# Optimization experiments

Measured on AMD Instinct MI355X. Metric: run time of the kernel, lower is better.

## Reference

```python
import jax, jax.numpy as jnp
import numpy as np

B_S, N_NODES, D_FEAT, N_HEADS, N_BLOCKS, AVG_DEG = 8, 4096, 128, 4, 32, 16
D_HID, N_CLASSES = 256, 16


def setup_inputs() -> dict:
    key = jax.random.key(0)
    ks = jax.random.split(key, 6)
    x = jax.random.normal(ks[0], (B_S, N_NODES, D_FEAT), jnp.float32)
    e_per = N_NODES * AVG_DEG
    src = jax.random.randint(ks[1], (B_S, e_per), 0, N_NODES)
    dst = jax.random.randint(ks[2], (B_S, e_per), 0, N_NODES)
    off = jnp.arange(B_S)[:, None] * N_NODES
    edge_index = jnp.stack([(src + off).reshape(-1), (dst + off).reshape(-1)], 0).astype(jnp.int32)
    W_rank = jax.random.normal(ks[3], (D_FEAT, N_HEADS), jnp.float32) / np.sqrt(D_FEAT)
    W1 = jax.random.normal(ks[4], (2 * D_FEAT, D_HID), jnp.float32) / np.sqrt(2.0 * D_FEAT)
    W_out = jax.random.normal(ks[5], (D_HID, N_CLASSES), jnp.float32) / np.sqrt(D_HID)
    return {"x": x, "W_rank": W_rank, "W1": W1, "W_out": W_out,
            "edge_index": edge_index, "j": N_BLOCKS}


def _forward(x, W_rank, W1, W_out, edge_index, j):
    b_s, n, d = x.shape
    h = W_rank.shape[1]
    k = n // j                      # block (subgraph) size; j*k == n
    Bp = h * b_s * j                # number of (head, graph, block) blocks
    src, dst = edge_index[0], edge_index[1]
    N = b_s * n
    x_flat = x.reshape(N, d)

    # GCN-normalized adjacency Ahat with self loops (selfloop=1)
    deg = jnp.ones(N, x.dtype).at[dst].add(1.0)
    w = jax.lax.rsqrt(deg[src] * deg[dst])

    def ahat_mv(v):  # Ahat @ v, v: [N, c]
        out = jnp.zeros_like(v).at[dst].add(w[:, None] * v[src])
        return out + v / deg[:, None]

    # app_adj: concat(x, Ahat @ x)
    x_appd = ahat_mv(x_flat)

    # ranking: linear scores + one propagation hop -> [b, h, n]
    scores = ahat_mv(x_flat @ W_rank)
    scores = scores.reshape(b_s, n, h).transpose(0, 2, 1)

    # perm_gen: full descending sort split into j blocks of k (sorted_idx [b,h,j,k])
    order = jnp.argsort(-scores, axis=-1)        # [b,h,n] node ids in rank order
    pos = jnp.argsort(order, axis=-1)            # inverse: node -> sorted slot
    sorted_scores = jnp.take_along_axis(scores, order, axis=-1)
    perm_val = jax.nn.sigmoid(sorted_scores).reshape(b_s, h, j, k)  # relaxed perm values
    sorted_blocks = order.reshape(b_s, h, j, k)
    # local target slot: rank of node id within each block (data-dependent perm)
    tgt = jnp.argsort(jnp.argsort(sorted_blocks, axis=-1), axis=-1)

    # gather features (with appended Ahat@x) into sorted block order
    feats = jnp.concatenate([x, x_appd.reshape(b_s, n, d)], -1)      # [b,n,2d]
    feats_sorted = feats[jnp.arange(b_s)[:, None, None], order]       # [b,h,n,2d]
    feats_in = feats_sorted.reshape(b_s, h, j, k, 2 * d).transpose(1, 0, 2, 3, 4).reshape(Bp, k, 2 * d)

    # edge masking per head: keep edges whose endpoints land in the same block,
    # remap to local slots -> dense block adjacency [Bp, k, k]
    b_e = src // n
    src_l, dst_l = src % n, dst % n
    heads = jnp.arange(h)
    pos_s = pos[b_e[:, None], heads[None, :], src_l[:, None]]   # [E,h]
    pos_d = pos[b_e[:, None], heads[None, :], dst_l[:, None]]
    blk_s, slot_s = pos_s // k, pos_s % k
    blk_d, slot_d = pos_d // k, pos_d % k
    keep = (blk_s == blk_d).astype(x.dtype)
    block_id = (heads[None, :] * b_s + b_e[:, None]) * j + blk_s  # (h,b,j) layout
    A = jnp.zeros((Bp, k, k), x.dtype).at[block_id, slot_s, slot_d].add(keep)

    # relaxed permutation matrix P[b', s, tgt_s] = v_s  (sub_size = 1)
    val_f = perm_val.transpose(1, 0, 2, 3).reshape(Bp, k)
    tgt_f = tgt.transpose(1, 0, 2, 3).reshape(Bp, k)
    P = jnp.zeros((Bp, k, k), x.dtype).at[
        jnp.arange(Bp)[:, None], jnp.arange(k)[None, :], tgt_f].set(val_f)

    # sparse_perm_2D: new_adj[tgt_s, tgt_t] += v_s * v_t * A[s, t]  ==  P^T A P
    A_perm = jnp.einsum('bsi,bst,btj->bij', P, A, P)
    X_perm = jnp.einsum('bsi,bsd->bid', P, feats_in)

    # cocn: one message-passing layer on permuted blocks + mean pool + head
    Hh = jax.nn.relu(jnp.einsum('bij,bjd->bid', A_perm, X_perm) @ W1)
    logits = Hh.mean(1) @ W_out                        # [Bp, C]
    logits = logits.reshape(h, b_s, j, -1).mean(0)     # head average -> [b, j, C]
    return jax.nn.log_softmax(logits, axis=-1)         # single-class task


def reference(x, W_rank, W1, W_out, edge_index, j):
    return _forward(x, W_rank, W1, W_out, edge_index, j)
```

## Files before the change

kernel.cpp:

```cpp
#include <hip/hip_runtime.h>
#include <cmath>

#define NB 8
#define NN 4096
#define DF 128
#define NH 4
#define NJ 32
#define NK 128
#define NTOT (NB*NN)
#define ETOT 524288
#define BPB (NH*NB*NJ)
#define DHID 256
#define NCLS 16
#define CAP_PB 96
#define CAP_BP 512

#define FP_SCALE 4194304.0
#define FP_INV   (1.0/4194304.0)

typedef short bf16x8 __attribute__((ext_vector_type(8)));
typedef float f32x4  __attribute__((ext_vector_type(4)));

__device__ __forceinline__ unsigned short f2bf(float f) {
    unsigned u = __float_as_uint(f);
    unsigned r = (u + 0x7FFFu + ((u >> 16) & 1u)) >> 16;
    return (unsigned short)r;
}
__device__ __forceinline__ float bf2f(unsigned short b) {
    unsigned u = ((unsigned)b) << 16;
    return __uint_as_float(u);
}

__device__ __forceinline__ unsigned long long make_key(float sc, int p) {
    unsigned u = __float_as_uint(sc);
    unsigned s = u ^ ((unsigned)((int)u >> 31) | 0x80000000u);
    return ((unsigned long long)(s ^ 0xFFFFFFFFu) << 12) | (unsigned)p;
}

__global__ void k0_init(int* deg_i, int* fill, int* fill2) {
    int t = blockIdx.x * blockDim.x + threadIdx.x;
    if (t < NTOT) { deg_i[t] = 0; fill2[t] = 0; }
    if (t < BPB) fill[t] = 0;
}

__global__ __launch_bounds__(256) void k1_deg_prep(const int* __restrict__ ei,
                                                   const float* __restrict__ x,
                                                   const float* __restrict__ W1,
                                                   const float* __restrict__ wr,
                                                   int* deg_i,
                                                   unsigned short* __restrict__ xbf,
                                                   unsigned short* __restrict__ w1t,
                                                   float* __restrict__ scores_pre) {
    int bid = blockIdx.x, tid = threadIdx.x;
    if (bid < 2048) {
        int e = bid * 256 + tid;
        atomicAdd(&deg_i[ei[ETOT + e]], 1);
    } else if (bid < 4096) {
        int idx = (bid - 2048) * 256 + tid;
        const float* sp = x + (size_t)idx * 8;
        float4 lo = *(const float4*)sp;
        float4 hi = *(const float4*)(sp + 4);
        unsigned short u[8] = {f2bf(lo.x), f2bf(lo.y), f2bf(lo.z), f2bf(lo.w),
                               f2bf(hi.x), f2bf(hi.y), f2bf(hi.z), f2bf(hi.w)};
        *(bf16x8*)(xbf + (size_t)idx * 8) = *(bf16x8*)u;
    } else if (bid < 4352) {
        int t = (bid - 4096) * 256 + tid;
        int k = t >> 8, n = t & 255;
        w1t[n * 256 + k] = f2bf(W1[k * DHID + n]);
    } else {
        int t = (bid - 4352) * 256 + tid;
        int g = t >> 2, hh = t & 3;
        const float* xr = x + (size_t)g * DF;
        double acc = 0.0;
        for (int d0 = 0; d0 < DF; ++d0) acc += (double)xr[d0] * (double)wr[d0 * NH + hh];
        scores_pre[t] = (float)acc;
    }
}

__global__ __launch_bounds__(256) void k_prep2(const int* __restrict__ deg_i,
                                               float* __restrict__ rdeg,
                                               int* __restrict__ nbase) {
    int bid = blockIdx.x, tid = threadIdx.x;
    if (bid < 128) {
        int t = bid * 256 + tid;
        rdeg[t] = 1.0f / sqrtf((float)(1 + deg_i[t]));
        return;
    }
    __shared__ int part[256];
    int base0 = tid * 128;
    int s = 0;
    for (int i = 0; i < 128; ++i) s += deg_i[base0 + i];
    part[tid] = s;
    __syncthreads();
    for (int off = 1; off < 256; off <<= 1) {
        int v = (tid >= off) ? part[tid - off] : 0;
        __syncthreads();
        part[tid] += v;
        __syncthreads();
    }
    int running = (tid == 0) ? 0 : part[tid - 1];
    for (int i = 0; i < 128; ++i) {
        nbase[base0 + i] = running;
        running += deg_i[base0 + i];
    }
    if (tid == 255) nbase[NTOT] = running;
}

__global__ void k3c_fill_csr(const int* __restrict__ ei, const int* __restrict__ nbase,
                             int* fill2, int* __restrict__ csr_src) {
    int e = blockIdx.x * blockDim.x + threadIdx.x;
    if (e >= ETOT) return;
    int s = ei[e], d = ei[ETOT + e];
    int slot = atomicAdd(&fill2[d], 1);
    csr_src[nbase[d] + slot] = s;
}

__global__ __launch_bounds__(256) void k4_gather(const int* __restrict__ csr_src,
                                                 const int* __restrict__ nbase,
                                                 const float* __restrict__ rdeg,
                                                 const float* __restrict__ x,
                                                 const float* __restrict__ scores_pre,
                                                 unsigned* __restrict__ xappbf,
                                                 int* __restrict__ iscore) {
    __shared__ unsigned long long nb[4][64];
    int bid = blockIdx.x;
    if (bid < 8192) {
        int swz = (bid & 7) * 1024 + (bid >> 3);
        int wid = threadIdx.x >> 6;
        int wv = swz * 4 + wid;
        int lane = threadIdx.x & 63;
        float rd = rdeg[wv];
        float2 v = ((const float2*)(x + (size_t)wv * DF))[lane];
        float acc0 = v.x * rd * rd, acc1 = v.y * rd * rd;
        int t0 = nbase[wv], t1 = nbase[wv + 1];
        int deg = t1 - t0;
        if (lane < deg && lane < 64) {
            int s = csr_src[t0 + lane];
            float w = rd * rdeg[s];
            nb[wid][lane] = ((unsigned long long)__float_as_uint(w) << 32)
                          | (unsigned)(s * DF);
        }
        int nfull = min(deg, 64);
#pragma unroll 4
        for (int t = 0; t < nfull; ++t) {
            unsigned long long e = nb[wid][t];
            float w = __uint_as_float((unsigned)(e >> 32));
            float2 u = ((const float2*)(x + (e & 0xFFFFFFFFu)))[lane];
            acc0 = fmaf(w, u.x, acc0);
            acc1 = fmaf(w, u.y, acc1);
        }
        for (int t = t0 + 64; t < t1; ++t) {
            int s = csr_src[t];
            float w = rd * rdeg[s];
            float2 u = ((const float2*)(x + (size_t)s * DF))[lane];
            acc0 = fmaf(w, u.x, acc0);
            acc1 = fmaf(w, u.y, acc1);
        }
        xappbf[(size_t)wv * 64 + lane] =
            (unsigned)f2bf(acc0) | ((unsigned)f2bf(acc1) << 16);
    } else {
        int t = (bid - 8192) * 256 + threadIdx.x;
        int d = t >> 2, hh = t & 3;
        float rdd = rdeg[d];
        int t0 = nbase[d], t1 = nbase[d + 1];
        int acc = 0;
        for (int e = t0; e < t1; ++e) {
            int s = csr_src[e];
            float w = rdeg[s] * rdd;
            double term = (double)(w * scores_pre[s * NH + hh]);
            acc += __double2int_rn(term * FP_SCALE);
        }
        iscore[t] = acc;
    }
}

__global__ __launch_bounds__(256) void kg_mfma(const unsigned short* __restrict__ xbf,
                                               const unsigned short* __restrict__ xappbf,
                                               const unsigned short* __restrict__ w1t,
                                               unsigned short* __restrict__ Gbf) {
    __shared__ __align__(16) unsigned short As[128 * 64];
    __shared__ __align__(16) unsigned short Bs[128 * 64];
    int bid = blockIdx.x;
    int m0 = (bid >> 1) * 128, n0 = (bid & 1) * 128;
    int tid = threadIdx.x, lane = tid & 63, wid = tid >> 6;
    int wr = wid >> 1, wc = wid & 1;
    f32x4 acc[4][4];
#pragma unroll
    for (int mi = 0; mi < 4; ++mi)
#pragma unroll
        for (int ni = 0; ni < 4; ++ni) acc[mi][ni] = f32x4{0.f, 0.f, 0.f, 0.f};

    for (int kk = 0; kk < 4; ++kk) {
        int k0 = kk * 64;
        const unsigned short* Asrc = (kk < 2) ? xbf : xappbf;
        int kbase = k0 & 127;
#pragma unroll
        for (int i = 0; i < 4; ++i) {
            int gi = tid + i * 256;
            int r = gi >> 3, c = gi & 7;
            int csrc = c ^ (r & 7);
            *(bf16x8*)&As[r * 64 + c * 8] =
                *(const bf16x8*)(Asrc + (size_t)(m0 + r) * DF + kbase + csrc * 8);
        }
#pragma unroll
        for (int i = 0; i < 4; ++i) {
            int gi = tid + i * 256;
            int r = gi >> 3, c = gi & 7;
            int csrc = c ^ (r & 7);
            *(bf16x8*)&Bs[r * 64 + c * 8] =
                *(const bf16x8*)(w1t + (size_t)(n0 + r) * 256 + k0 + csrc * 8);
        }
        __syncthreads();
#pragma unroll
        for (int ks = 0; ks < 2; ++ks) {
            bf16x8 af[4], bfr[4];
#pragma unroll
            for (int mi = 0; mi < 4; ++mi) {
                int r = wr * 64 + mi * 16 + (lane & 15);
                int gl = ks * 4 + (lane >> 4);
                af[mi] = *(const bf16x8*)&As[r * 64 + (gl ^ (r & 7)) * 8];
            }
#pragma unroll
            for (int ni = 0; ni < 4; ++ni) {
                int r = wc * 64 + ni * 16 + (lane & 15);
                int gl = ks * 4 + (lane >> 4);
                bfr[ni] = *(const bf16x8*)&Bs[r * 64 + (gl ^ (r & 7)) * 8];
            }
#pragma unroll
            for (int mi = 0; mi < 4; ++mi)
#pragma unroll
                for (int ni = 0; ni < 4; ++ni)
                    acc[mi][ni] = __builtin_amdgcn_mfma_f32_16x16x32_bf16(
                        af[mi], bfr[ni], acc[mi][ni], 0, 0, 0);
        }
        __syncthreads();
    }
#pragma unroll
    for (int mi = 0; mi < 4; ++mi) {
        int rbase = m0 + wr * 64 + mi * 16 + (lane >> 4) * 4;
#pragma unroll
        for (int ni = 0; ni < 4; ++ni) {
            int col = n0 + wc * 64 + ni * 16 + (lane & 15);
#pragma unroll
            for (int j = 0; j < 4; ++j)
                Gbf[(size_t)(rbase + j) * DHID + col] = f2bf(acc[mi][ni][j]);
        }
    }
}

__global__ __launch_bounds__(256) void k5a_chunk(const float* __restrict__ scores_pre,
                                                 const int* __restrict__ iscore,
                                                 const int* __restrict__ deg_i,
                                                 unsigned long long* __restrict__ sorted64) {
    __shared__ unsigned long long sk[512];
    int blk = blockIdx.x;
    int seg = blk >> 3, chunk = blk & 7;
    int b = seg >> 2, hh = seg & 3;
    int tid = threadIdx.x;
    for (int i = tid; i < 512; i += 256) {
        int p = chunk * 512 + i;
        int g = b * NN + p;
        float dg = (float)(1 + deg_i[g]);
        float sc = scores_pre[g * NH + hh] / dg + (float)((double)iscore[g * NH + hh] * FP_INV);
        sk[i] = make_key(sc, p);
    }
    __syncthreads();
    for (int size = 2; size <= 512; size <<= 1) {
        for (int stride = size >> 1; stride > 0; stride >>= 1) {
            for (int p = tid; p < 512; p += 256) {
                int q = p ^ stride;
                if (q > p) {
                    unsigned long long kp = sk[p], kq = sk[q];
                    bool before_qp = (kq < kp);
                    bool asc = ((p & size) == 0);
                    if (asc ? before_qp : !before_qp) { sk[p] = kq; sk[q] = kp; }
                }
            }
            __syncthreads();
        }
    }
    for (int i = tid; i < 512; i += 256)
        sorted64[seg * NN + chunk * 512 + i] = sk[i];
}

__global__ __launch_bounds__(256) void k5b_rank(const unsigned long long* __restrict__ sorted64,
                                                int* __restrict__ order, int* __restrict__ pos,
                                                float* __restrict__ val) {
    int t = blockIdx.x * 256 + threadIdx.x;
    int seg = t >> 12, i = t & 4095;
    int chunk = i >> 9, slot = i & 511;
    const unsigned long long* segp = sorted64 + (size_t)seg * NN;
    unsigned long long k = segp[chunk * 512 + slot];
    int rank = slot;
#pragma unroll
    for (int c = 0; c < 8; ++c) {
        if (c == chunk) continue;
        const unsigned long long* cp = segp + c * 512;
        int lo = 0, hi = 512;
        while (lo < hi) { int mid = (lo + hi) >> 1; lo = (cp[mid] < k) ? mid + 1 : lo; hi = (cp[mid] < k) ? hi : mid; }
        rank += lo;
    }
    int p = (int)(k & 4095u);
    pos[seg * NN + p] = rank;
    order[seg * NN + rank] = p;
    unsigned s = (unsigned)(k >> 12) ^ 0xFFFFFFFFu;
    unsigned u = s ^ (((int)s >= 0) ? 0xFFFFFFFFu : 0x80000000u);
    float sc = __uint_as_float(u);
    val[seg * NN + rank] = 1.0f / (1.0f + expf(-sc));
}

__global__ __launch_bounds__(256) void k56_tgt_bin(const int* __restrict__ order,
                                                   const int* __restrict__ ei,
                                                   const int* __restrict__ pos,
                                                   int* __restrict__ tgt,
                                                   int* fill, unsigned* __restrict__ elist) {
    __shared__ unsigned short pos_l[NN];
    __shared__ unsigned buf[NJ][CAP_PB];
    __shared__ int lcnt[NJ];
    __shared__ int gbase[NJ];
    int bid = blockIdx.x, tid = threadIdx.x;
    if (bid < 512) {
        int* o = (int*)pos_l;
        int base = bid * 256;
        o[tid] = order[base + tid];
        __syncthreads();
        int g0 = tid & ~127;
        int me = o[tid];
        int r = 0;
#pragma unroll 16
        for (int s2 = 0; s2 < 128; ++s2) r += (o[g0 + s2] < me) ? 1 : 0;
        tgt[base + tid] = r;
        return;
    }
    int blkid = bid - 512;
    int ph = blkid >> 3, part = blkid & 7;
    int b = ph >> 2, hh = ph & 3;
    for (int i = tid; i < NN; i += 256) pos_l[i] = (unsigned short)pos[ph * NN + i];
    if (tid < NJ) lcnt[tid] = 0;
    __syncthreads();
    int ebase = b * 65536 + part * 8192;
    for (int i = tid; i < 8192; i += 256) {
        int e = ebase + i;
        int s = ei[e], d = ei[ETOT + e];
        int ps = pos_l[s & 4095], pd = pos_l[d & 4095];
        if ((ps >> 7) == (pd >> 7)) {
            int blk = ps >> 7;
            int slot = atomicAdd(&lcnt[blk], 1);
            if (slot < CAP_PB)
                buf[blk][slot] = (unsigned)((ps & 127) | ((pd & 127) << 16));
        }
    }
    __syncthreads();
    if (tid < NJ) {
        int n = min(lcnt[tid], CAP_PB);
        lcnt[tid] = n;
        gbase[tid] = atomicAdd(&fill[((hh * NB + b) * NJ) + tid], n);
    }
    __syncthreads();
    for (int t = tid; t < NJ * CAP_PB; t += 256) {
        int blk = t / CAP_PB, i = t % CAP_PB;
        if (i < lcnt[blk]) {
            int g0 = gbase[blk] + i;
            if (g0 < CAP_BP) {
                int bpid = ((hh * NB + b) * NJ) + blk;
                elist[bpid * CAP_BP + g0] = buf[blk][i];
            }
        }
    }
}

__global__ __launch_bounds__(256) void k9_block(const unsigned short* __restrict__ Gbf,
                                                const int* __restrict__ order,
                                                const float* __restrict__ val,
                                                const int* __restrict__ tgt,
                                                const int* __restrict__ fill,
                                                const unsigned* __restrict__ elist,
                                                const float* __restrict__ Wo,
                                                float* __restrict__ logits_bp) {
    __shared__ float val_s[NK];
    __shared__ int   node_s[NK];
    __shared__ int   tgt_s[NK];
    __shared__ int   rcnt[NK];
    __shared__ int   rend[NK];
    __shared__ int   rfill[NK];
    __shared__ unsigned es_meta[CAP_BP];
    __shared__ float    es_coef[CAP_BP];
    __shared__ float hvec[DHID];
    int i0 = blockIdx.x;
    int xcd = i0 & 7, r0 = i0 >> 3;
    int hh = r0 >> 5, blk = r0 & 31, b = xcd;
    int bp = (hh * NB + b) * NJ + blk;
    int ph = (b << 2) | hh;
    int tid = threadIdx.x;
    if (tid < NK) {
        int p = blk * NK + tid;
        node_s[tid] = order[ph * NN + p];
        val_s[tid]  = val[ph * NN + p];
        tgt_s[tid]  = tgt[ph * NN + p];
        rcnt[tid] = 0; rfill[tid] = 0;
    }
    __syncthreads();
    int e0 = bp * CAP_BP;
    int ne = min(fill[bp], CAP_BP);
    for (int t = tid; t < ne; t += 256)
        atomicAdd(&rcnt[tgt_s[elist[e0 + t] & 0xffff]], 1);
    __syncthreads();
    if (tid < NK) rend[tid] = rcnt[tid];
    __syncthreads();
    for (int off = 1; off < NK; off <<= 1) {
        int v = 0;
        if (tid < NK && tid >= off) v = rend[tid - off];
        __syncthreads();
        if (tid < NK) rend[tid] += v;
        __syncthreads();
    }
    for (int t = tid; t < ne; t += 256) {
        unsigned ent = elist[e0 + t];
        int ss = ent & 0xffff, sd = ent >> 16;
        int row = tgt_s[ss];
        int slot = atomicAdd(&rfill[row], 1);
        int p0 = rend[row] - rcnt[row] + slot;
        es_meta[p0] = ((unsigned)row << 16) | (unsigned)node_s[sd];
        es_coef[p0] = val_s[ss] * val_s[sd] * val_s[sd];
    }
    __syncthreads();
    size_t gb = (size_t)b * NN * DHID + tid;
    float hsum = 0.f, m = 0.f;
    int prev = -1;
#pragma unroll 4
    for (int i = 0; i < ne; ++i) {
        unsigned md = es_meta[i];
        int row = (int)(md >> 16);
        float g = bf2f(Gbf[gb + (size_t)(md & 0xffffu) * DHID]);
        float c = es_coef[i];
        bool flush = (row != prev);
        hsum += flush ? fmaxf(m, 0.f) : 0.f;
        m = flush ? c * g : fmaf(c, g, m);
        prev = row;
    }
    hsum += fmaxf(m, 0.f);
    hvec[tid] = hsum * (1.0f / NK);
    __syncthreads();
    if (tid < NCLS) {
        float s = 0.f;
        for (int q = 0; q < DHID; ++q) s = fmaf(hvec[q], Wo[q * NCLS + tid], s);
        logits_bp[bp * NCLS + tid] = s;
    }
}

__global__ void k10_final(const float* __restrict__ logits_bp, float* __restrict__ out) {
    int t = threadIdx.x;
    int b = t >> 5, blk = t & 31;
    float v[NCLS];
#pragma unroll
    for (int c = 0; c < NCLS; ++c) {
        float s = 0.f;
        for (int hh = 0; hh < NH; ++hh)
            s += logits_bp[(((hh * NB + b) * NJ) + blk) * NCLS + c];
        v[c] = s * 0.25f;
    }
    float mx = v[0];
#pragma unroll
    for (int c = 1; c < NCLS; ++c) mx = fmaxf(mx, v[c]);
    float se = 0.f;
#pragma unroll
    for (int c = 0; c < NCLS; ++c) se += expf(v[c] - mx);
    float lse = logf(se);
#pragma unroll
    for (int c = 0; c < NCLS; ++c) out[t * NCLS + c] = v[c] - mx - lse;
}

extern "C" void kernel_launch(void* const* d_in, const int* in_sizes, int n_in,
                              void* d_out, int out_size, void* d_ws, size_t ws_size,
                              hipStream_t stream) {
    const float* x  = (const float*)d_in[0];
    const float* wr = (const float*)d_in[1];
    const float* W1 = (const float*)d_in[2];
    const float* Wo = (const float*)d_in[3];
    const int*   ei = (const int*)d_in[4];

    char* ws = (char*)d_ws;
    int*      deg_i      = (int*)(ws + 0);
    float*    rdeg       = (float*)(ws + 131072);
    float*    scores_pre = (float*)(ws + 262144);
    int*      iscore     = (int*)(ws + 786432);
    unsigned short* xbf  = (unsigned short*)(ws + 1310720);
    unsigned* xappbf     = (unsigned*)(ws + 9699328);
    unsigned short* Gbf  = (unsigned short*)(ws + 18087936);
    int*      order      = (int*)(ws + 51642368);
    int*      pos        = (int*)(ws + 52166656);
    int*      tgt        = (int*)(ws + 52690944);
    float*    val        = (float*)(ws + 53215232);
    int*      fill       = (int*)(ws + 53743616);
    int*      csr_src    = (int*)(ws + 53755904);
    unsigned short* w1t  = (unsigned short*)(ws + 55853056);
    unsigned* elist      = (unsigned*)(ws + 53755904);
    float*    logits_bp  = (float*)(ws + 62144512);
    int*      nbase      = (int*)(ws + 62210048);
    int*      fill2      = (int*)(ws + 62341184);
    unsigned long long* sorted64 = (unsigned long long*)(ws + 62472256);

    k0_init<<<128, 256, 0, stream>>>(deg_i, fill, fill2);
    k1_deg_prep<<<4864, 256, 0, stream>>>(ei, x, W1, wr, deg_i, xbf, w1t, scores_pre);
    k_prep2<<<129, 256, 0, stream>>>(deg_i, rdeg, nbase);
    k3c_fill_csr<<<2048, 256, 0, stream>>>(ei, nbase, fill2, csr_src);
    k4_gather<<<8704, 256, 0, stream>>>(csr_src, nbase, rdeg, x, scores_pre, xappbf, iscore);
    kg_mfma<<<512, 256, 0, stream>>>(xbf, (const unsigned short*)xappbf, w1t, Gbf);
    k5a_chunk<<<256, 256, 0, stream>>>(scores_pre, iscore, deg_i, sorted64);
    k5b_rank<<<512, 256, 0, stream>>>(sorted64, order, pos, val);
    k56_tgt_bin<<<768, 256, 0, stream>>>(order, ei, pos, tgt, fill, elist);
    k9_block<<<BPB, 256, 0, stream>>>(Gbf, order, val, tgt, fill, elist, Wo, logits_bp);
    k10_final<<<1, 256, 0, stream>>>(logits_bp, (float*)d_out);
}
```

Before: 199.1 us.

## Gather bf16 features, swizzle edge blocks, merge GEMM with chunk sort launch

Result: faster. 183.8 us (-7.7%).

```diff
diff --git a/kernel.cpp b/kernel.cpp
--- a/kernel.cpp
+++ b/kernel.cpp
@@ -53,7 +53,7 @@
                                                    float* __restrict__ scores_pre) {
     int bid = blockIdx.x, tid = threadIdx.x;
     if (bid < 2048) {
-        int e = bid * 256 + tid;
+        int e = (bid & 7) * 65536 + (bid >> 3) * 256 + tid;
         atomicAdd(&deg_i[ei[ETOT + e]], 1);
     } else if (bid < 4096) {
         int idx = (bid - 2048) * 256 + tid;
@@ -108,8 +108,8 @@
 
 __global__ void k3c_fill_csr(const int* __restrict__ ei, const int* __restrict__ nbase,
                              int* fill2, int* __restrict__ csr_src) {
-    int e = blockIdx.x * blockDim.x + threadIdx.x;
-    if (e >= ETOT) return;
+    int bid = blockIdx.x;
+    int e = (bid & 7) * 65536 + (bid >> 3) * 256 + threadIdx.x;
     int s = ei[e], d = ei[ETOT + e];
     int slot = atomicAdd(&fill2[d], 1);
     csr_src[nbase[d] + slot] = s;
@@ -119,6 +119,7 @@
                                                  const int* __restrict__ nbase,
                                                  const float* __restrict__ rdeg,
                                                  const float* __restrict__ x,
+                                                 const unsigned short* __restrict__ xbf,
                                                  const float* __restrict__ scores_pre,
                                                  unsigned* __restrict__ xappbf,
                                                  int* __restrict__ iscore) {
@@ -145,16 +146,16 @@
         for (int t = 0; t < nfull; ++t) {
             unsigned long long e = nb[wid][t];
             float w = __uint_as_float((unsigned)(e >> 32));
-            float2 u = ((const float2*)(x + (e & 0xFFFFFFFFu)))[lane];
-            acc0 = fmaf(w, u.x, acc0);
-            acc1 = fmaf(w, u.y, acc1);
+            unsigned u = ((const unsigned*)(xbf + (e & 0xFFFFFFFFu)))[lane];
+            acc0 = fmaf(w, bf2f((unsigned short)(u & 0xffff)), acc0);
+            acc1 = fmaf(w, bf2f((unsigned short)(u >> 16)), acc1);
         }
         for (int t = t0 + 64; t < t1; ++t) {
             int s = csr_src[t];
             float w = rd * rdeg[s];
-            float2 u = ((const float2*)(x + (size_t)s * DF))[lane];
-            acc0 = fmaf(w, u.x, acc0);
-            acc1 = fmaf(w, u.y, acc1);
+            unsigned u = ((const unsigned*)(xbf + (size_t)s * DF))[lane];
+            acc0 = fmaf(w, bf2f((unsigned short)(u & 0xffff)), acc0);
+            acc1 = fmaf(w, bf2f((unsigned short)(u >> 16)), acc1);
         }
         xappbf[(size_t)wv * 64 + lane] =
             (unsigned)f2bf(acc0) | ((unsigned)f2bf(acc1) << 16);
@@ -174,89 +175,89 @@
     }
 }
 
-__global__ __launch_bounds__(256) void kg_mfma(const unsigned short* __restrict__ xbf,
-                                               const unsigned short* __restrict__ xappbf,
-                                               const unsigned short* __restrict__ w1t,
-                                               unsigned short* __restrict__ Gbf) {
-    __shared__ __align__(16) unsigned short As[128 * 64];
-    __shared__ __align__(16) unsigned short Bs[128 * 64];
-    int bid = blockIdx.x;
-    int m0 = (bid >> 1) * 128, n0 = (bid & 1) * 128;
-    int tid = threadIdx.x, lane = tid & 63, wid = tid >> 6;
-    int wr = wid >> 1, wc = wid & 1;
-    f32x4 acc[4][4];
-#pragma unroll
-    for (int mi = 0; mi < 4; ++mi)
-#pragma unroll
-        for (int ni = 0; ni < 4; ++ni) acc[mi][ni] = f32x4{0.f, 0.f, 0.f, 0.f};
-
-    for (int kk = 0; kk < 4; ++kk) {
-        int k0 = kk * 64;
-        const unsigned short* Asrc = (kk < 2) ? xbf : xappbf;
-        int kbase = k0 & 127;
-#pragma unroll
-        for (int i = 0; i < 4; ++i) {
-            int gi = tid + i * 256;
-            int r = gi >> 3, c = gi & 7;
-            int csrc = c ^ (r & 7);
-            *(bf16x8*)&As[r * 64 + c * 8] =
-                *(const bf16x8*)(Asrc + (size_t)(m0 + r) * DF + kbase + csrc * 8);
-        }
-#pragma unroll
-        for (int i = 0; i < 4; ++i) {
-            int gi = tid + i * 256;
-            int r = gi >> 3, c = gi & 7;
-            int csrc = c ^ (r & 7);
-            *(bf16x8*)&Bs[r * 64 + c * 8] =
-                *(const bf16x8*)(w1t + (size_t)(n0 + r) * 256 + k0 + csrc * 8);
-        }
-        __syncthreads();
-#pragma unroll
-        for (int ks = 0; ks < 2; ++ks) {
-            bf16x8 af[4], bfr[4];
-#pragma unroll
-            for (int mi = 0; mi < 4; ++mi) {
-                int r = wr * 64 + mi * 16 + (lane & 15);
-                int gl = ks * 4 + (lane >> 4);
-                af[mi] = *(const bf16x8*)&As[r * 64 + (gl ^ (r & 7)) * 8];
+__global__ __launch_bounds__(256) void kg5a(const unsigned short* __restrict__ xbf,
+                                            const unsigned short* __restrict__ xappbf,
+                                            const unsigned short* __restrict__ w1t,
+                                            unsigned short* __restrict__ Gbf,
+                                            const float* __restrict__ scores_pre,
+                                            const int* __restrict__ iscore,
+                                            const int* __restrict__ deg_i,
+                                            unsigned long long* __restrict__ sorted64) {
+    __shared__ __align__(16) unsigned char smem[32768];
+    int bid = blockIdx.x, tid = threadIdx.x;
+    if (bid < 512) {
+        unsigned short* As = (unsigned short*)smem;
+        unsigned short* Bs = (unsigned short*)(smem + 16384);
+        int m0 = (bid >> 1) * 128, n0 = (bid & 1) * 128;
+        int lane = tid & 63, wid = tid >> 6;
+        int wr = wid >> 1, wc = wid & 1;
+        f32x4 acc[4][4];
+#pragma unroll
+        for (int mi = 0; mi < 4; ++mi)
+#pragma unroll
+            for (int ni = 0; ni < 4; ++ni) acc[mi][ni] = f32x4{0.f, 0.f, 0.f, 0.f};
+        for (int kk = 0; kk < 4; ++kk) {
+            int k0 = kk * 64;
+            const unsigned short* Asrc = (kk < 2) ? xbf : xappbf;
+            int kbase = k0 & 127;
+#pragma unroll
+            for (int i = 0; i < 4; ++i) {
+                int gi = tid + i * 256;
+                int r = gi >> 3, c = gi & 7;
+                int csrc = c ^ (r & 7);
+                *(bf16x8*)&As[r * 64 + c * 8] =
+                    *(const bf16x8*)(Asrc + (size_t)(m0 + r) * DF + kbase + csrc * 8);
             }
 #pragma unroll
+            for (int i = 0; i < 4; ++i) {
+                int gi = tid + i * 256;
+                int r = gi >> 3, c = gi & 7;
+                int csrc = c ^ (r & 7);
+                *(bf16x8*)&Bs[r * 64 + c * 8] =
+                    *(const bf16x8*)(w1t + (size_t)(n0 + r) * 256 + k0 + csrc * 8);
+            }
+            __syncthreads();
+#pragma unroll
+            for (int ks = 0; ks < 2; ++ks) {
+                bf16x8 af[4], bfr[4];
+#pragma unroll
+                for (int mi = 0; mi < 4; ++mi) {
+                    int r = wr * 64 + mi * 16 + (lane & 15);
+                    int gl = ks * 4 + (lane >> 4);
+                    af[mi] = *(const bf16x8*)&As[r * 64 + (gl ^ (r & 7)) * 8];
+                }
+#pragma unroll
+                for (int ni = 0; ni < 4; ++ni) {
+                    int r = wc * 64 + ni * 16 + (lane & 15);
+                    int gl = ks * 4 + (lane >> 4);
+                    bfr[ni] = *(const bf16x8*)&Bs[r * 64 + (gl ^ (r & 7)) * 8];
+                }
+#pragma unroll
+                for (int mi = 0; mi < 4; ++mi)
+#pragma unroll
+                    for (int ni = 0; ni < 4; ++ni)
+                        acc[mi][ni] = __builtin_amdgcn_mfma_f32_16x16x32_bf16(
+                            af[mi], bfr[ni], acc[mi][ni], 0, 0, 0);
+            }
+            __syncthreads();
+        }
+#pragma unroll
+        for (int mi = 0; mi < 4; ++mi) {
+            int rbase = m0 + wr * 64 + mi * 16 + (lane >> 4) * 4;
+#pragma unroll
             for (int ni = 0; ni < 4; ++ni) {
-                int r = wc * 64 + ni * 16 + (lane & 15);
-                int gl = ks * 4 + (lane >> 4);
-                bfr[ni] = *(const bf16x8*)&Bs[r * 64 + (gl ^ (r & 7)) * 8];
+                int col = n0 + wc * 64 + ni * 16 + (lane & 15);
+#pragma unroll
+                for (int j = 0; j < 4; ++j)
+                    Gbf[(size_t)(rbase + j) * DHID + col] = f2bf(acc[mi][ni][j]);
             }
-#pragma unroll
-            for (int mi = 0; mi < 4; ++mi)
-#pragma unroll
-                for (int ni = 0; ni < 4; ++ni)
-                    acc[mi][ni] = __builtin_amdgcn_mfma_f32_16x16x32_bf16(
-                        af[mi], bfr[ni], acc[mi][ni], 0, 0, 0);
-        }
-        __syncthreads();
-    }
-#pragma unroll
-    for (int mi = 0; mi < 4; ++mi) {
-        int rbase = m0 + wr * 64 + mi * 16 + (lane >> 4) * 4;
-#pragma unroll
-        for (int ni = 0; ni < 4; ++ni) {
-            int col = n0 + wc * 64 + ni * 16 + (lane & 15);
-#pragma unroll
-            for (int j = 0; j < 4; ++j)
-                Gbf[(size_t)(rbase + j) * DHID + col] = f2bf(acc[mi][ni][j]);
-        }
-    }
-}
-
-__global__ __launch_bounds__(256) void k5a_chunk(const float* __restrict__ scores_pre,
-                                                 const int* __restrict__ iscore,
-                                                 const int* __restrict__ deg_i,
-                                                 unsigned long long* __restrict__ sorted64) {
-    __shared__ unsigned long long sk[512];
-    int blk = blockIdx.x;
+        }
+        return;
+    }
+    unsigned long long* sk = (unsigned long long*)smem;
+    int blk = bid - 512;
     int seg = blk >> 3, chunk = blk & 7;
     int b = seg >> 2, hh = seg & 3;
-    int tid = threadIdx.x;
     for (int i = tid; i < 512; i += 256) {
         int p = chunk * 512 + i;
         int g = b * NN + p;
@@ -504,9 +505,9 @@
     k1_deg_prep<<<4864, 256, 0, stream>>>(ei, x, W1, wr, deg_i, xbf, w1t, scores_pre);
     k_prep2<<<129, 256, 0, stream>>>(deg_i, rdeg, nbase);
     k3c_fill_csr<<<2048, 256, 0, stream>>>(ei, nbase, fill2, csr_src);
-    k4_gather<<<8704, 256, 0, stream>>>(csr_src, nbase, rdeg, x, scores_pre, xappbf, iscore);
-    kg_mfma<<<512, 256, 0, stream>>>(xbf, (const unsigned short*)xappbf, w1t, Gbf);
-    k5a_chunk<<<256, 256, 0, stream>>>(scores_pre, iscore, deg_i, sorted64);
+    k4_gather<<<8704, 256, 0, stream>>>(csr_src, nbase, rdeg, x, xbf, scores_pre, xappbf, iscore);
+    kg5a<<<768, 256, 0, stream>>>(xbf, (const unsigned short*)xappbf, w1t, Gbf,
+                                  scores_pre, iscore, deg_i, sorted64);
     k5b_rank<<<512, 256, 0, stream>>>(sorted64, order, pos, val);
     k56_tgt_bin<<<768, 256, 0, stream>>>(order, ei, pos, tgt, fill, elist);
     k9_block<<<BPB, 256, 0, stream>>>(Gbf, order, val, tgt, fill, elist, Wo, logits_bp);
```
